# Kernel optimization log

Measured on AMD Instinct MI355X. Metric: run time of the kernel, lower is better.

The kernel has to match this reference:

```python
import jax, jax.numpy as jnp
import numpy as np

DELTA_COEFF = 1.0
CLAMP_MIN = 1e-3  # hardcoded in original clamp(min=0.001)


def setup_inputs() -> dict:
    key = jax.random.key(0)
    k1, k2, k3 = jax.random.split(key, 3)
    B, N, F_in, F_out = 2, 1024, 128, 64
    x = jax.random.normal(k1, (B, N, F_in), dtype=jnp.float32)
    adj = jax.random.uniform(k2, (B, N, N), dtype=jnp.float32)
    weight = jax.random.normal(k3, (F_in, F_out), dtype=jnp.float32) * (1.0 / np.sqrt(F_in))
    bias = jnp.zeros((F_out,), dtype=jnp.float32)
    return {"x": x, "adj": adj, "weight": weight, "bias": bias}


def reference(x, adj, weight, bias):
    # x: [B,N,F_in], adj: [B,N,N]
    x = x @ weight  # [B,N,F_out]
    B, N, _ = adj.shape
    # pairwise L1 distance: [B,N,N]
    abs_diff = jnp.sum(jnp.abs(x[:, :, None, :] - x[:, None, :, :]), axis=-1)
    mod_adj = adj / jnp.maximum(abs_diff, CLAMP_MIN)
    deg = jnp.sum(mod_adj, axis=-1)  # [B,N]
    # Laplacian L = D - A~ ; then I - delta * L
    lap = jnp.zeros_like(mod_adj).at[:, jnp.arange(N), jnp.arange(N)].set(deg) - mod_adj
    mod = jnp.eye(N, dtype=x.dtype) - DELTA_COEFF * lap
    out = jnp.matmul(mod, x) + bias
    return out
```

## Files before the change

kernel.cpp:

```cpp
#include <hip/hip_runtime.h>
#include <hip/hip_fp16.h>


#define JS 16
#define HSTR 72

typedef _Float16 half4_t __attribute__((ext_vector_type(4)));
typedef _Float16 half8_t __attribute__((ext_vector_type(8)));
typedef float    f32x4_t __attribute__((ext_vector_type(4)));

__global__ __launch_bounds__(256) void gemm_xw(const float* __restrict__ x,
                                               const float* __restrict__ w,
                                               float* __restrict__ xw,
                                               __half* __restrict__ xwh,
                                               __half* __restrict__ xwt) {
    __shared__ float ws_[128 * 64];
    __shared__ float xs[8 * 132];
    __shared__ __half ts[8 * 64];
    const int tid = threadIdx.x;
    const int r0  = blockIdx.x * 8;

#pragma unroll
    for (int e = tid; e < 2048; e += 256)
        ((float4*)ws_)[e] = ((const float4*)w)[e];
    {
        int row = tid >> 5, c = tid & 31;
        float4 v = *(const float4*)&x[(size_t)(r0 + row) * 128 + c * 4];
        *(float4*)&xs[row * 132 + c * 4] = v;
    }
    __syncthreads();

    const int rl = tid >> 5;
    const int fg = tid & 31;
    float2 acc = {0.f, 0.f};
#pragma unroll
    for (int k4 = 0; k4 < 32; ++k4) {
        float4 xv = *(const float4*)&xs[rl * 132 + k4 * 4];
        const float* xp = &xv.x;
#pragma unroll
        for (int m = 0; m < 4; ++m) {
            float2 wv = *(const float2*)&ws_[(k4 * 4 + m) * 64 + 2 * fg];
            acc.x += xp[m] * wv.x; acc.y += xp[m] * wv.y;
        }
    }
    size_t o = (size_t)(r0 + rl) * 64 + 2 * fg;
    *(float2*)&xw[o] = acc;
    __half2 h2 = __floats2half2_rn(acc.x, acc.y);
    *(__half2*)&xwh[o] = h2;
    *(__half2*)&ts[rl * 64 + 2 * fg] = h2;
    __syncthreads();

    if (tid < 64) {
        const int f = tid;
        const int b = r0 >> 10;
        const int n0 = r0 & 1023;
        __half hv[8];
#pragma unroll
        for (int r = 0; r < 8; ++r) hv[r] = ts[r * 64 + f];
        *(half8_t*)&xwt[((size_t)(b * 64 + f)) * 1024 + n0] = *(half8_t*)hv;
    }
}

template <bool ATOMIC>
__global__ __launch_bounds__(256) void fused_gtv(const __half* __restrict__ xwh,
                                                 const __half* __restrict__ xwt,
                                                 const float* __restrict__ adj,
                                                 __half* __restrict__ part,
                                                 float* __restrict__ aout,
                                                 float* __restrict__ pdeg) {
    __shared__ __half xih[64 * HSTR];
    __shared__ __half xjh[64 * HSTR];
    __shared__ __half xjt[64 * HSTR];
    __shared__ __half wt [64 * HSTR];

    const int tid = threadIdx.x;
    const int bx  = blockIdx.x;
    const int js  = bx & 15;
    const int it  = (bx >> 4) & 15;
    const int b   = bx >> 8;
    const int i0  = it * 64;
    const int j0  = js * 64;

    const __half* xhb = xwh + (size_t)b * 65536;
    const __half* xtb = xwt + (size_t)b * 65536;
    const float*  adjb = adj + (size_t)b * 1048576;

    const int ty = tid >> 4;
    const int tx = tid & 15;

    float4 av[4];
#pragma unroll
    for (int r = 0; r < 4; ++r)
        av[r] = *(const float4*)&adjb[(size_t)(i0 + 4 * ty + r) * 1024 + j0 + 4 * tx];

#pragma unroll
    for (int e = tid; e < 512; e += 256) {
        int row = e >> 3, cb = e & 7;
        int sc = ((cb ^ ((row >> 2) & 7)) << 3);
        float4 vi = *(const float4*)&xhb[(i0 + row) * 64 + cb * 8];
        *(float4*)&xih[row * HSTR + sc] = vi;
        float4 vj = *(const float4*)&xhb[(j0 + row) * 64 + cb * 8];
        *(float4*)&xjh[row * HSTR + sc] = vj;
        float4 vt = *(const float4*)&xtb[row * 1024 + j0 + cb * 8];
        *(float4*)&xjt[row * HSTR + cb * 8] = vt;
    }
    __syncthreads();

    __half2 acc[4][4];
#pragma unroll
    for (int r = 0; r < 4; ++r)
#pragma unroll
        for (int q = 0; q < 4; ++q) acc[r][q] = __floats2half2_rn(0.f, 0.f);

#pragma unroll
    for (int c = 0; c < 8; ++c) {
        const int ca = ((c ^ (ty & 7)) << 3);
        const int cb = ((c ^ (tx & 7)) << 3);
        float4 a[4], bb[4];
#pragma unroll
        for (int r = 0; r < 4; ++r)
            a[r] = *(const float4*)&xih[(4 * ty + r) * HSTR + ca];
#pragma unroll
        for (int q = 0; q < 4; ++q)
            bb[q] = *(const float4*)&xjh[(4 * tx + q) * HSTR + cb];
#pragma unroll
        for (int r = 0; r < 4; ++r) {
            const __half2* pa = (const __half2*)&a[r];
#pragma unroll
            for (int q = 0; q < 4; ++q) {
                const __half2* pb = (const __half2*)&bb[q];
#pragma unroll
                for (int m = 0; m < 4; ++m)
                    acc[r][q] = __hadd2(acc[r][q], __habs2(__hsub2(pa[m], pb[m])));
            }
        }
    }

    float dsum[4];
#pragma unroll
    for (int r = 0; r < 4; ++r) {
        const int gi = i0 + 4 * ty + r;
        float wv[4];
        dsum[r] = 0.f;
#pragma unroll
        for (int q = 0; q < 4; ++q) {
            float d = __low2float(acc[r][q]) + __high2float(acc[r][q]);
            float inv = __builtin_amdgcn_rcpf(fmaxf(d, 1e-3f));
            float v = (&av[r].x)[q] * inv;
            wv[q] = (gi == j0 + 4 * tx + q) ? 0.f : v;
            dsum[r] += wv[q];
        }
        float2 packed;
        ((__half2*)&packed)[0] = __floats2half2_rn(wv[0], wv[1]);
        ((__half2*)&packed)[1] = __floats2half2_rn(wv[2], wv[3]);
        *(float2*)&wt[(4 * ty + r) * HSTR + 4 * tx] = packed;
    }
#pragma unroll
    for (int r = 0; r < 4; ++r) {
#pragma unroll
        for (int m = 1; m < 16; m <<= 1)
            dsum[r] += __shfl_xor(dsum[r], m, 16);
    }
    if (tx == 0) {
#pragma unroll
        for (int r = 0; r < 4; ++r) {
            if (ATOMIC) atomicAdd(&pdeg[b * 1024 + i0 + 4 * ty + r], dsum[r]);
            else pdeg[(js * 2 + b) * 1024 + i0 + 4 * ty + r] = dsum[r];
        }
    }
    __syncthreads();

    const int wv_  = tid >> 6;
    const int lane = tid & 63;
    const int quad = lane >> 4;
    const int l15  = lane & 15;

    f32x4_t c[4] = {{0,0,0,0},{0,0,0,0},{0,0,0,0},{0,0,0,0}};
    half8_t a0 = *(half8_t*)&wt[(wv_ * 16 + l15) * HSTR + quad * 8];
    half8_t a1 = *(half8_t*)&wt[(wv_ * 16 + l15) * HSTR + 32 + quad * 8];
#pragma unroll
    for (int n = 0; n < 4; ++n) {
        half8_t b0 = *(half8_t*)&xjt[(n * 16 + l15) * HSTR + quad * 8];
        half8_t b1 = *(half8_t*)&xjt[(n * 16 + l15) * HSTR + 32 + quad * 8];
        c[n] = __builtin_amdgcn_mfma_f32_16x16x32_f16(a0, b0, c[n], 0, 0, 0);
        c[n] = __builtin_amdgcn_mfma_f32_16x16x32_f16(a1, b1, c[n], 0, 0, 0);
    }

    if (ATOMIC) {
#pragma unroll
        for (int n = 0; n < 4; ++n)
#pragma unroll
            for (int r = 0; r < 4; ++r) {
                int row = wv_ * 16 + quad * 4 + r;
                atomicAdd(&aout[((size_t)b * 1024 + i0 + row) * 64 + n * 16 + l15], c[n][r]);
            }
    } else {
        const size_t slot = (size_t)(js * 2 + b) * 65536;
#pragma unroll
        for (int n = 0; n < 4; ++n)
#pragma unroll
            for (int r = 0; r < 4; ++r) {
                int row = wv_ * 16 + quad * 4 + r;
                part[slot + (i0 + row) * 64 + n * 16 + l15] = __float2half(c[n][r]);
            }
    }
}

__global__ __launch_bounds__(256) void finish_gtv_v2(const float* __restrict__ xw,
                                                     const __half* __restrict__ part,
                                                     const float* __restrict__ pdeg,
                                                     const float* __restrict__ bias,
                                                     float* __restrict__ out) {
    int idx2 = blockIdx.x * 256 + threadIdx.x;
    int f2 = idx2 & 31;
    int r  = idx2 >> 5;
    int b  = r >> 10;
    int n  = r & 1023;

    float2 s = {0.f, 0.f};
    float dgs = 0.f;
    const __half2* p2 = (const __half2*)part;
#pragma unroll
    for (int js = 0; js < JS; ++js) {
        int sl = js * 2 + b;
        __half2 h = p2[(size_t)sl * 32768 + n * 32 + f2];
        float2 f = __half22float2(h);
        s.x += f.x; s.y += f.y;
        dgs += pdeg[sl * 1024 + n];
    }
    float2 xv = ((const float2*)xw)[idx2];
    float2 bv = ((const float2*)bias)[f2];
    float id = 1.f - dgs;
    float2 o;
    o.x = s.x + id * xv.x + bv.x;
    o.y = s.y + id * xv.y + bv.y;
    ((float2*)out)[idx2] = o;
}

__global__ __launch_bounds__(256) void finish_gtv_atomic(const float* __restrict__ xw,
                                                         const float* __restrict__ pdeg,
                                                         const float* __restrict__ bias,
                                                         float* __restrict__ out) {
    int idx = blockIdx.x * 256 + threadIdx.x;
    int f = idx & 63;
    int r = idx >> 6;
    out[idx] = out[idx] + (1.f - pdeg[r]) * xw[idx] + bias[f];
}

extern "C" void kernel_launch(void* const* d_in, const int* in_sizes, int n_in,
                              void* d_out, int out_size, void* d_ws, size_t ws_size,
                              hipStream_t stream) {
    const float* x    = (const float*)d_in[0];
    const float* adj  = (const float*)d_in[1];
    const float* w    = (const float*)d_in[2];
    const float* bias = (const float*)d_in[3];
    float* out = (float*)d_out;

    char* wsb = (char*)d_ws;
    float*  xw   = (float*)wsb;
    __half* xwh  = (__half*)(wsb + 512 * 1024);
    __half* xwt  = (__half*)(wsb + 768 * 1024);
    float*  pdeg = (float*)(wsb + 1024 * 1024);
    __half* part = (__half*)(wsb + 1152 * 1024);
    const size_t NEED = 1152 * 1024 + (size_t)32 * 65536 * 2;

    gemm_xw<<<256, 256, 0, stream>>>(x, w, xw, xwh, xwt);

    if (ws_size >= NEED) {
        fused_gtv<false><<<512, 256, 0, stream>>>(xwh, xwt, adj, part, nullptr, pdeg);
        finish_gtv_v2<<<256, 256, 0, stream>>>(xw, part, pdeg, bias, out);
    } else {
        hipMemsetAsync(out, 0, 2 * 1024 * 64 * sizeof(float), stream);
        hipMemsetAsync(pdeg, 0, 2 * 1024 * sizeof(float), stream);
        fused_gtv<true><<<512, 256, 0, stream>>>(xwh, xwt, adj, nullptr, out, pdeg);
        finish_gtv_atomic<<<512, 256, 0, stream>>>(xw, pdeg, bias, out);
    }
}
```

Measured before the change: 81.61 us.

## Fuse final reduction into gtv kernel via last-block election counter

The partial-sum reduction and output epilogue move into the main fused kernel. An atomic per-row-tile counter elects the last of the 16 column blocks to sum the fp16 partials and degree partials and write the output. This removes a separate kernel launch and its dependency gap. It adds a threadfence/atomic handshake and relies on the counter in workspace starting at a multiple of 16, since it is never reset explicitly. The atomic fallback path is split into its own kernel.

```diff
diff --git a/kernel.cpp b/kernel.cpp
--- a/kernel.cpp
+++ b/kernel.cpp
@@ -61,13 +61,15 @@
     }
 }
 
-template <bool ATOMIC>
-__global__ __launch_bounds__(256) void fused_gtv(const __half* __restrict__ xwh,
-                                                 const __half* __restrict__ xwt,
-                                                 const float* __restrict__ adj,
-                                                 __half* __restrict__ part,
-                                                 float* __restrict__ aout,
-                                                 float* __restrict__ pdeg) {
+__global__ __launch_bounds__(256) void fused_gtv_fin(const __half* __restrict__ xwh,
+                                                     const __half* __restrict__ xwt,
+                                                     const float* __restrict__ adj,
+                                                     __half* __restrict__ part,
+                                                     float* __restrict__ pdeg,
+                                                     const float* __restrict__ xw,
+                                                     const float* __restrict__ bias,
+                                                     float* __restrict__ out,
+                                                     unsigned* __restrict__ done) {
     __shared__ __half xih[64 * HSTR];
     __shared__ __half xjh[64 * HSTR];
     __shared__ __half xjt[64 * HSTR];
@@ -163,10 +165,8 @@
     }
     if (tx == 0) {
 #pragma unroll
-        for (int r = 0; r < 4; ++r) {
-            if (ATOMIC) atomicAdd(&pdeg[b * 1024 + i0 + 4 * ty + r], dsum[r]);
-            else pdeg[(js * 2 + b) * 1024 + i0 + 4 * ty + r] = dsum[r];
-        }
+        for (int r = 0; r < 4; ++r)
+            pdeg[(js * 2 + b) * 1024 + i0 + 4 * ty + r] = dsum[r];
     }
     __syncthreads();
 
@@ -186,55 +186,184 @@
         c[n] = __builtin_amdgcn_mfma_f32_16x16x32_f16(a1, b1, c[n], 0, 0, 0);
     }
 
-    if (ATOMIC) {
-#pragma unroll
-        for (int n = 0; n < 4; ++n)
-#pragma unroll
-            for (int r = 0; r < 4; ++r) {
-                int row = wv_ * 16 + quad * 4 + r;
-                atomicAdd(&aout[((size_t)b * 1024 + i0 + row) * 64 + n * 16 + l15], c[n][r]);
+    const size_t slot = (size_t)(js * 2 + b) * 65536;
+#pragma unroll
+    for (int n = 0; n < 4; ++n)
+#pragma unroll
+        for (int r = 0; r < 4; ++r) {
+            int row = wv_ * 16 + quad * 4 + r;
+            part[slot + (i0 + row) * 64 + n * 16 + l15] = __float2half(c[n][r]);
+        }
+
+    __syncthreads();
+    __shared__ int elect;
+    if (tid == 0) {
+        __threadfence();
+        unsigned old = atomicAdd(&done[b * 16 + it], 1u);
+        elect = ((old & 15u) == 15u);
+    }
+    __syncthreads();
+    if (!elect) return;
+    __threadfence();
+
+    const float2*  xw2   = (const float2*)xw;
+    const float2*  bias2 = (const float2*)bias;
+    const __half2* p2    = (const __half2*)part;
+    float2*        out2  = (float2*)out;
+#pragma unroll 2
+    for (int k = 0; k < 8; ++k) {
+        int e   = tid + k * 256;
+        int row = e >> 5;
+        int f2  = e & 31;
+        int n   = i0 + row;
+        size_t gr = (size_t)b * 1024 + n;
+        float sx = 0.f, sy = 0.f, dg = 0.f;
+#pragma unroll
+        for (int q = 0; q < JS; ++q) {
+            int sl = q * 2 + b;
+            __half2 h = p2[(size_t)sl * 32768 + (size_t)n * 32 + f2];
+            float2 f = __half22float2(h);
+            sx += f.x; sy += f.y;
+            dg += pdeg[sl * 1024 + n];
+        }
+        float2 xv = xw2[gr * 32 + f2];
+        float2 bv = bias2[f2];
+        float id = 1.f - dg;
+        float2 o;
+        o.x = sx + id * xv.x + bv.x;
+        o.y = sy + id * xv.y + bv.y;
+        out2[gr * 32 + f2] = o;
+    }
+}
+
+__global__ __launch_bounds__(256) void fused_gtv_atomic(const __half* __restrict__ xwh,
+                                                        const __half* __restrict__ xwt,
+                                                        const float* __restrict__ adj,
+                                                        float* __restrict__ aout,
+                                                        float* __restrict__ pdeg) {
+    __shared__ __half xih[64 * HSTR];
+    __shared__ __half xjh[64 * HSTR];
+    __shared__ __half xjt[64 * HSTR];
+    __shared__ __half wt [64 * HSTR];
+
+    const int tid = threadIdx.x;
+    const int bx  = blockIdx.x;
+    const int js  = bx & 15;
+    const int it  = (bx >> 4) & 15;
+    const int b   = bx >> 8;
+    const int i0  = it * 64;
+    const int j0  = js * 64;
+
+    const __half* xhb = xwh + (size_t)b * 65536;
+    const __half* xtb = xwt + (size_t)b * 65536;
+    const float*  adjb = adj + (size_t)b * 1048576;
+
+    const int ty = tid >> 4;
+    const int tx = tid & 15;
+
+    float4 av[4];
+#pragma unroll
+    for (int r = 0; r < 4; ++r)
+        av[r] = *(const float4*)&adjb[(size_t)(i0 + 4 * ty + r) * 1024 + j0 + 4 * tx];
+
+#pragma unroll
+    for (int e = tid; e < 512; e += 256) {
+        int row = e >> 3, cb = e & 7;
+        int sc = ((cb ^ ((row >> 2) & 7)) << 3);
+        float4 vi = *(const float4*)&xhb[(i0 + row) * 64 + cb * 8];
+        *(float4*)&xih[row * HSTR + sc] = vi;
+        float4 vj = *(const float4*)&xhb[(j0 + row) * 64 + cb * 8];
+        *(float4*)&xjh[row * HSTR + sc] = vj;
+        float4 vt = *(const float4*)&xtb[row * 1024 + j0 + cb * 8];
+        *(float4*)&xjt[row * HSTR + cb * 8] = vt;
+    }
+    __syncthreads();
+
+    __half2 acc[4][4];
+#pragma unroll
+    for (int r = 0; r < 4; ++r)
+#pragma unroll
+        for (int q = 0; q < 4; ++q) acc[r][q] = __floats2half2_rn(0.f, 0.f);
+
+#pragma unroll
+    for (int c = 0; c < 8; ++c) {
+        const int ca = ((c ^ (ty & 7)) << 3);
+        const int cb = ((c ^ (tx & 7)) << 3);
+        float4 a[4], bb[4];
+#pragma unroll
+        for (int r = 0; r < 4; ++r)
+            a[r] = *(const float4*)&xih[(4 * ty + r) * HSTR + ca];
+#pragma unroll
+        for (int q = 0; q < 4; ++q)
+            bb[q] = *(const float4*)&xjh[(4 * tx + q) * HSTR + cb];
+#pragma unroll
+        for (int r = 0; r < 4; ++r) {
+            const __half2* pa = (const __half2*)&a[r];
+#pragma unroll
+            for (int q = 0; q < 4; ++q) {
+                const __half2* pb = (const __half2*)&bb[q];
+#pragma unroll
+                for (int m = 0; m < 4; ++m)
+                    acc[r][q] = __hadd2(acc[r][q], __habs2(__hsub2(pa[m], pb[m])));
             }
-    } else {
-        const size_t slot = (size_t)(js * 2 + b) * 65536;
-#pragma unroll
-        for (int n = 0; n < 4; ++n)
-#pragma unroll
-            for (int r = 0; r < 4; ++r) {
-                int row = wv_ * 16 + quad * 4 + r;
-                part[slot + (i0 + row) * 64 + n * 16 + l15] = __float2half(c[n][r]);
-            }
-    }
-}
-
-__global__ __launch_bounds__(256) void finish_gtv_v2(const float* __restrict__ xw,
-                                                     const __half* __restrict__ part,
-                                                     const float* __restrict__ pdeg,
-                                                     const float* __restrict__ bias,
-                                                     float* __restrict__ out) {
-    int idx2 = blockIdx.x * 256 + threadIdx.x;
-    int f2 = idx2 & 31;
-    int r  = idx2 >> 5;
-    int b  = r >> 10;
-    int n  = r & 1023;
-
-    float2 s = {0.f, 0.f};
-    float dgs = 0.f;
-    const __half2* p2 = (const __half2*)part;
-#pragma unroll
-    for (int js = 0; js < JS; ++js) {
-        int sl = js * 2 + b;
-        __half2 h = p2[(size_t)sl * 32768 + n * 32 + f2];
-        float2 f = __half22float2(h);
-        s.x += f.x; s.y += f.y;
-        dgs += pdeg[sl * 1024 + n];
-    }
-    float2 xv = ((const float2*)xw)[idx2];
-    float2 bv = ((const float2*)bias)[f2];
-    float id = 1.f - dgs;
-    float2 o;
-    o.x = s.x + id * xv.x + bv.x;
-    o.y = s.y + id * xv.y + bv.y;
-    ((float2*)out)[idx2] = o;
+        }
+    }
+
+    float dsum[4];
+#pragma unroll
+    for (int r = 0; r < 4; ++r) {
+        const int gi = i0 + 4 * ty + r;
+        float wv[4];
+        dsum[r] = 0.f;
+#pragma unroll
+        for (int q = 0; q < 4; ++q) {
+            float d = __low2float(acc[r][q]) + __high2float(acc[r][q]);
+            float inv = __builtin_amdgcn_rcpf(fmaxf(d, 1e-3f));
+            float v = (&av[r].x)[q] * inv;
+            wv[q] = (gi == j0 + 4 * tx + q) ? 0.f : v;
+            dsum[r] += wv[q];
+        }
+        float2 packed;
+        ((__half2*)&packed)[0] = __floats2half2_rn(wv[0], wv[1]);
+        ((__half2*)&packed)[1] = __floats2half2_rn(wv[2], wv[3]);
+        *(float2*)&wt[(4 * ty + r) * HSTR + 4 * tx] = packed;
+    }
+#pragma unroll
+    for (int r = 0; r < 4; ++r) {
+#pragma unroll
+        for (int m = 1; m < 16; m <<= 1)
+            dsum[r] += __shfl_xor(dsum[r], m, 16);
+    }
+    if (tx == 0) {
+#pragma unroll
+        for (int r = 0; r < 4; ++r)
+            atomicAdd(&pdeg[b * 1024 + i0 + 4 * ty + r], dsum[r]);
+    }
+    __syncthreads();
+
+    const int wv_  = tid >> 6;
+    const int lane = tid & 63;
+    const int quad = lane >> 4;
+    const int l15  = lane & 15;
+
+    f32x4_t c[4] = {{0,0,0,0},{0,0,0,0},{0,0,0,0},{0,0,0,0}};
+    half8_t a0 = *(half8_t*)&wt[(wv_ * 16 + l15) * HSTR + quad * 8];
+    half8_t a1 = *(half8_t*)&wt[(wv_ * 16 + l15) * HSTR + 32 + quad * 8];
+#pragma unroll
+    for (int n = 0; n < 4; ++n) {
+        half8_t b0 = *(half8_t*)&xjt[(n * 16 + l15) * HSTR + quad * 8];
+        half8_t b1 = *(half8_t*)&xjt[(n * 16 + l15) * HSTR + 32 + quad * 8];
+        c[n] = __builtin_amdgcn_mfma_f32_16x16x32_f16(a0, b0, c[n], 0, 0, 0);
+        c[n] = __builtin_amdgcn_mfma_f32_16x16x32_f16(a1, b1, c[n], 0, 0, 0);
+    }
+
+#pragma unroll
+    for (int n = 0; n < 4; ++n)
+#pragma unroll
+        for (int r = 0; r < 4; ++r) {
+            int row = wv_ * 16 + quad * 4 + r;
+            atomicAdd(&aout[((size_t)b * 1024 + i0 + row) * 64 + n * 16 + l15], c[n][r]);
+        }
 }
 
 __global__ __launch_bounds__(256) void finish_gtv_atomic(const float* __restrict__ xw,
@@ -257,22 +386,23 @@
     float* out = (float*)d_out;
 
     char* wsb = (char*)d_ws;
-    float*  xw   = (float*)wsb;
-    __half* xwh  = (__half*)(wsb + 512 * 1024);
-    __half* xwt  = (__half*)(wsb + 768 * 1024);
-    float*  pdeg = (float*)(wsb + 1024 * 1024);
-    __half* part = (__half*)(wsb + 1152 * 1024);
-    const size_t NEED = 1152 * 1024 + (size_t)32 * 65536 * 2;
+    float*    xw   = (float*)wsb;
+    __half*   xwh  = (__half*)(wsb + 512 * 1024);
+    __half*   xwt  = (__half*)(wsb + 768 * 1024);
+    float*    pdeg = (float*)(wsb + 1024 * 1024);
+    __half*   part = (__half*)(wsb + 1152 * 1024);
+    unsigned* done = (unsigned*)(wsb + 5248 * 1024);
+    const size_t NEED = 5248 * 1024 + 128;
 
     gemm_xw<<<256, 256, 0, stream>>>(x, w, xw, xwh, xwt);
 
     if (ws_size >= NEED) {
-        fused_gtv<false><<<512, 256, 0, stream>>>(xwh, xwt, adj, part, nullptr, pdeg);
-        finish_gtv_v2<<<256, 256, 0, stream>>>(xw, part, pdeg, bias, out);
+        fused_gtv_fin<<<512, 256, 0, stream>>>(xwh, xwt, adj, part, pdeg,
+                                               xw, bias, out, done);
     } else {
         hipMemsetAsync(out, 0, 2 * 1024 * 64 * sizeof(float), stream);
         hipMemsetAsync(pdeg, 0, 2 * 1024 * sizeof(float), stream);
-        fused_gtv<true><<<512, 256, 0, stream>>>(xwh, xwt, adj, nullptr, out, pdeg);
+        fused_gtv_atomic<<<512, 256, 0, stream>>>(xwh, xwt, adj, out, pdeg);
         finish_gtv_atomic<<<512, 256, 0, stream>>>(xw, pdeg, bias, out);
     }
 }
```

Result: slower. 104.4 us (+27.9%).

## Fuse distance, degree, aggregation and epilogue into one row-block kernel

Applied to the files above, without the earlier changes.

Replaces the 64x64 tiled pairwise kernel plus reduction/finish kernel with a single kernel where each block owns four output rows across all 1024 columns. Degree sums and the MFMA aggregation are completed in-block, removing the fp16 partial buffer, the extra launch and the atomic fallback. In exchange, each thread reads neighbor feature rows directly from global memory with little reuse, and the MFMA tiles are padded from 4 to 16 rows, wasting most of the matrix work.

```diff
diff --git a/kernel.cpp b/kernel.cpp
--- a/kernel.cpp
+++ b/kernel.cpp
@@ -2,10 +2,8 @@
 #include <hip/hip_fp16.h>
 
 
-#define JS 16
-#define HSTR 72
+#define WSTR 1032
 
-typedef _Float16 half4_t __attribute__((ext_vector_type(4)));
 typedef _Float16 half8_t __attribute__((ext_vector_type(8)));
 typedef float    f32x4_t __attribute__((ext_vector_type(4)));
 
@@ -61,50 +59,44 @@
     }
 }
 
-template <bool ATOMIC>
-__global__ __launch_bounds__(256) void fused_gtv(const __half* __restrict__ xwh,
-                                                 const __half* __restrict__ xwt,
-                                                 const float* __restrict__ adj,
-                                                 __half* __restrict__ part,
-                                                 float* __restrict__ aout,
-                                                 float* __restrict__ pdeg) {
-    __shared__ __half xih[64 * HSTR];
-    __shared__ __half xjh[64 * HSTR];
-    __shared__ __half xjt[64 * HSTR];
-    __shared__ __half wt [64 * HSTR];
+__global__ __launch_bounds__(256) void fused_rows(const __half* __restrict__ xwh,
+                                                  const __half* __restrict__ xwt,
+                                                  const float* __restrict__ adj,
+                                                  const float* __restrict__ xw,
+                                                  const float* __restrict__ bias,
+                                                  float* __restrict__ out) {
+    __shared__ __half xih[4 * 64];
+    __shared__ __half wt[16 * WSTR];
+    __shared__ float  ps[4 * 68];
+    __shared__ float  dpart[16];
 
-    const int tid = threadIdx.x;
-    const int bx  = blockIdx.x;
-    const int js  = bx & 15;
-    const int it  = (bx >> 4) & 15;
-    const int b   = bx >> 8;
-    const int i0  = it * 64;
-    const int j0  = js * 64;
+    const int tid  = threadIdx.x;
+    const int bx   = blockIdx.x;
+    const int b    = bx >> 8;
+    const int i0   = (bx & 255) * 4;
+    const int w_   = tid >> 6;
+    const int lane = tid & 63;
 
-    const __half* xhb = xwh + (size_t)b * 65536;
-    const __half* xtb = xwt + (size_t)b * 65536;
-    const float*  adjb = adj + (size_t)b * 1048576;
+    const __half* xb = xwh + (size_t)b * 65536;
 
-    const int ty = tid >> 4;
-    const int tx = tid & 15;
+    if (tid < 32) {
+        int row = tid >> 3, cb = tid & 7;
+        *(float4*)&xih[row * 64 + cb * 8] =
+            *(const float4*)&xb[(i0 + row) * 64 + cb * 8];
+    }
+    {
+        float4 z = {0.f, 0.f, 0.f, 0.f};
+        float4* wz = (float4*)&wt[4 * WSTR];
+#pragma unroll 2
+        for (int e = tid; e < 1548; e += 256) wz[e] = z;
+    }
+    __syncthreads();
 
     float4 av[4];
 #pragma unroll
     for (int r = 0; r < 4; ++r)
-        av[r] = *(const float4*)&adjb[(size_t)(i0 + 4 * ty + r) * 1024 + j0 + 4 * tx];
-
-#pragma unroll
-    for (int e = tid; e < 512; e += 256) {
-        int row = e >> 3, cb = e & 7;
-        int sc = ((cb ^ ((row >> 2) & 7)) << 3);
-        float4 vi = *(const float4*)&xhb[(i0 + row) * 64 + cb * 8];
-        *(float4*)&xih[row * HSTR + sc] = vi;
-        float4 vj = *(const float4*)&xhb[(j0 + row) * 64 + cb * 8];
-        *(float4*)&xjh[row * HSTR + sc] = vj;
-        float4 vt = *(const float4*)&xtb[row * 1024 + j0 + cb * 8];
-        *(float4*)&xjt[row * HSTR + cb * 8] = vt;
-    }
-    __syncthreads();
+        av[r] = *(const float4*)&adj[(size_t)b * 1048576 +
+                                     (size_t)(i0 + r) * 1024 + 4 * tid];
 
     __half2 acc[4][4];
 #pragma unroll
@@ -113,22 +105,18 @@
         for (int q = 0; q < 4; ++q) acc[r][q] = __floats2half2_rn(0.f, 0.f);
 
 #pragma unroll
-    for (int c = 0; c < 8; ++c) {
-        const int ca = ((c ^ (ty & 7)) << 3);
-        const int cb = ((c ^ (tx & 7)) << 3);
-        float4 a[4], bb[4];
+    for (int q = 0; q < 4; ++q) {
+        float4 bj[8];
 #pragma unroll
-        for (int r = 0; r < 4; ++r)
-            a[r] = *(const float4*)&xih[(4 * ty + r) * HSTR + ca];
+        for (int cb = 0; cb < 8; ++cb)
+            bj[cb] = *(const float4*)&xb[(size_t)(4 * tid + q) * 64 + cb * 8];
 #pragma unroll
-        for (int q = 0; q < 4; ++q)
-            bb[q] = *(const float4*)&xjh[(4 * tx + q) * HSTR + cb];
+        for (int cb = 0; cb < 8; ++cb) {
+            const __half2* pb = (const __half2*)&bj[cb];
 #pragma unroll
-        for (int r = 0; r < 4; ++r) {
-            const __half2* pa = (const __half2*)&a[r];
-#pragma unroll
-            for (int q = 0; q < 4; ++q) {
-                const __half2* pb = (const __half2*)&bb[q];
+            for (int r = 0; r < 4; ++r) {
+                float4 a = *(const float4*)&xih[r * 64 + cb * 8];
+                const __half2* pa = (const __half2*)&a;
 #pragma unroll
                 for (int m = 0; m < 4; ++m)
                     acc[r][q] = __hadd2(acc[r][q], __habs2(__hsub2(pa[m], pb[m])));
@@ -136,115 +124,60 @@
         }
     }
 
-    float dsum[4];
+    float dsum[4] = {0.f, 0.f, 0.f, 0.f};
 #pragma unroll
     for (int r = 0; r < 4; ++r) {
-        const int gi = i0 + 4 * ty + r;
+        const int gi = i0 + r;
         float wv[4];
-        dsum[r] = 0.f;
 #pragma unroll
         for (int q = 0; q < 4; ++q) {
             float d = __low2float(acc[r][q]) + __high2float(acc[r][q]);
             float inv = __builtin_amdgcn_rcpf(fmaxf(d, 1e-3f));
             float v = (&av[r].x)[q] * inv;
-            wv[q] = (gi == j0 + 4 * tx + q) ? 0.f : v;
+            wv[q] = (gi == 4 * tid + q) ? 0.f : v;
             dsum[r] += wv[q];
         }
         float2 packed;
         ((__half2*)&packed)[0] = __floats2half2_rn(wv[0], wv[1]);
         ((__half2*)&packed)[1] = __floats2half2_rn(wv[2], wv[3]);
-        *(float2*)&wt[(4 * ty + r) * HSTR + 4 * tx] = packed;
+        *(float2*)&wt[r * WSTR + 4 * tid] = packed;
     }
 #pragma unroll
     for (int r = 0; r < 4; ++r) {
 #pragma unroll
-        for (int m = 1; m < 16; m <<= 1)
-            dsum[r] += __shfl_xor(dsum[r], m, 16);
+        for (int m = 1; m < 64; m <<= 1)
+            dsum[r] += __shfl_xor(dsum[r], m, 64);
     }
-    if (tx == 0) {
+    if (lane == 0) {
 #pragma unroll
-        for (int r = 0; r < 4; ++r) {
-            if (ATOMIC) atomicAdd(&pdeg[b * 1024 + i0 + 4 * ty + r], dsum[r]);
-            else pdeg[(js * 2 + b) * 1024 + i0 + 4 * ty + r] = dsum[r];
-        }
+        for (int r = 0; r < 4; ++r) dpart[w_ * 4 + r] = dsum[r];
     }
     __syncthreads();
 
-    const int wv_  = tid >> 6;
-    const int lane = tid & 63;
     const int quad = lane >> 4;
     const int l15  = lane & 15;
+    const __half* bt = xwt + (size_t)b * 65536 + (size_t)(w_ * 16 + l15) * 1024;
 
-    f32x4_t c[4] = {{0,0,0,0},{0,0,0,0},{0,0,0,0},{0,0,0,0}};
-    half8_t a0 = *(half8_t*)&wt[(wv_ * 16 + l15) * HSTR + quad * 8];
-    half8_t a1 = *(half8_t*)&wt[(wv_ * 16 + l15) * HSTR + 32 + quad * 8];
+    f32x4_t c = {0.f, 0.f, 0.f, 0.f};
+#pragma unroll 8
+    for (int kc = 0; kc < 32; ++kc) {
+        half8_t af = *(const half8_t*)&wt[l15 * WSTR + kc * 32 + quad * 8];
+        half8_t bf = *(const half8_t*)&bt[kc * 32 + quad * 8];
+        c = __builtin_amdgcn_mfma_f32_16x16x32_f16(af, bf, c, 0, 0, 0);
+    }
+    if (quad == 0) {
 #pragma unroll
-    for (int n = 0; n < 4; ++n) {
-        half8_t b0 = *(half8_t*)&xjt[(n * 16 + l15) * HSTR + quad * 8];
-        half8_t b1 = *(half8_t*)&xjt[(n * 16 + l15) * HSTR + 32 + quad * 8];
-        c[n] = __builtin_amdgcn_mfma_f32_16x16x32_f16(a0, b0, c[n], 0, 0, 0);
-        c[n] = __builtin_amdgcn_mfma_f32_16x16x32_f16(a1, b1, c[n], 0, 0, 0);
+        for (int r = 0; r < 4; ++r) ps[r * 68 + w_ * 16 + l15] = c[r];
     }
+    __syncthreads();
 
-    if (ATOMIC) {
-#pragma unroll
-        for (int n = 0; n < 4; ++n)
-#pragma unroll
-            for (int r = 0; r < 4; ++r) {
-                int row = wv_ * 16 + quad * 4 + r;
-                atomicAdd(&aout[((size_t)b * 1024 + i0 + row) * 64 + n * 16 + l15], c[n][r]);
-            }
-    } else {
-        const size_t slot = (size_t)(js * 2 + b) * 65536;
-#pragma unroll
-        for (int n = 0; n < 4; ++n)
-#pragma unroll
-            for (int r = 0; r < 4; ++r) {
-                int row = wv_ * 16 + quad * 4 + r;
-                part[slot + (i0 + row) * 64 + n * 16 + l15] = __float2half(c[n][r]);
-            }
+    {
+        int row = tid >> 6;
+        int f   = tid & 63;
+        float deg = dpart[row] + dpart[4 + row] + dpart[8 + row] + dpart[12 + row];
+        size_t o = ((size_t)b * 1024 + i0 + row) * 64 + f;
+        out[o] = (1.f - deg) * xw[o] + ps[row * 68 + f] + bias[f];
     }
-}
-
-__global__ __launch_bounds__(256) void finish_gtv_v2(const float* __restrict__ xw,
-                                                     const __half* __restrict__ part,
-                                                     const float* __restrict__ pdeg,
-                                                     const float* __restrict__ bias,
-                                                     float* __restrict__ out) {
-    int idx2 = blockIdx.x * 256 + threadIdx.x;
-    int f2 = idx2 & 31;
-    int r  = idx2 >> 5;
-    int b  = r >> 10;
-    int n  = r & 1023;
-
-    float2 s = {0.f, 0.f};
-    float dgs = 0.f;
-    const __half2* p2 = (const __half2*)part;
-#pragma unroll
-    for (int js = 0; js < JS; ++js) {
-        int sl = js * 2 + b;
-        __half2 h = p2[(size_t)sl * 32768 + n * 32 + f2];
-        float2 f = __half22float2(h);
-        s.x += f.x; s.y += f.y;
-        dgs += pdeg[sl * 1024 + n];
-    }
-    float2 xv = ((const float2*)xw)[idx2];
-    float2 bv = ((const float2*)bias)[f2];
-    float id = 1.f - dgs;
-    float2 o;
-    o.x = s.x + id * xv.x + bv.x;
-    o.y = s.y + id * xv.y + bv.y;
-    ((float2*)out)[idx2] = o;
-}
-
-__global__ __launch_bounds__(256) void finish_gtv_atomic(const float* __restrict__ xw,
-                                                         const float* __restrict__ pdeg,
-                                                         const float* __restrict__ bias,
-                                                         float* __restrict__ out) {
-    int idx = blockIdx.x * 256 + threadIdx.x;
-    int f = idx & 63;
-    int r = idx >> 6;
-    out[idx] = out[idx] + (1.f - pdeg[r]) * xw[idx] + bias[f];
 }
 
 extern "C" void kernel_launch(void* const* d_in, const int* in_sizes, int n_in,
@@ -257,22 +190,10 @@
     float* out = (float*)d_out;
 
     char* wsb = (char*)d_ws;
-    float*  xw   = (float*)wsb;
-    __half* xwh  = (__half*)(wsb + 512 * 1024);
-    __half* xwt  = (__half*)(wsb + 768 * 1024);
-    float*  pdeg = (float*)(wsb + 1024 * 1024);
-    __half* part = (__half*)(wsb + 1152 * 1024);
-    const size_t NEED = 1152 * 1024 + (size_t)32 * 65536 * 2;
+    float*  xw  = (float*)wsb;
+    __half* xwh = (__half*)(wsb + 512 * 1024);
+    __half* xwt = (__half*)(wsb + 768 * 1024);
 
     gemm_xw<<<256, 256, 0, stream>>>(x, w, xw, xwh, xwt);
-
-    if (ws_size >= NEED) {
-        fused_gtv<false><<<512, 256, 0, stream>>>(xwh, xwt, adj, part, nullptr, pdeg);
-        finish_gtv_v2<<<256, 256, 0, stream>>>(xw, part, pdeg, bias, out);
-    } else {
-        hipMemsetAsync(out, 0, 2 * 1024 * 64 * sizeof(float), stream);
-        hipMemsetAsync(pdeg, 0, 2 * 1024 * sizeof(float), stream);
-        fused_gtv<true><<<512, 256, 0, stream>>>(xwh, xwt, adj, nullptr, out, pdeg);
-        finish_gtv_atomic<<<512, 256, 0, stream>>>(xw, pdeg, bias, out);
-    }
+    fused_rows<<<512, 256, 0, stream>>>(xwh, xwt, adj, xw, bias, out);
 }
```

Measured after the change: 86.31 us. 1.06x slower.

## Fuse three kernels into one cooperative launch with grid syncs

Applied to the files above, without the earlier changes.

Merges the projection GEMM, the fused pairwise-L1/Laplacian kernel and the finish reduction into one cooperative kernel separated by grid.sync, with a union of shared memory buffers. It falls back to the three separate launches if the cooperative launch fails. It also replaces the half2 abs with a sign-bit mask in the L1 accumulation. The aim is to remove the overhead and tail gaps of two kernel launches, at the cost of grid barriers and a larger shared-memory footprint per block, which may reduce occupancy.

```diff
diff --git a/kernel.cpp b/kernel.cpp
--- a/kernel.cpp
+++ b/kernel.cpp
@@ -1,25 +1,31 @@
 #include <hip/hip_runtime.h>
 #include <hip/hip_fp16.h>
+#include <hip/hip_cooperative_groups.h>
+
+namespace cg = cooperative_groups;
 
 
 #define JS 16
 #define HSTR 72
 
-typedef _Float16 half4_t __attribute__((ext_vector_type(4)));
 typedef _Float16 half8_t __attribute__((ext_vector_type(8)));
+typedef _Float16 h2_t    __attribute__((ext_vector_type(2)));
 typedef float    f32x4_t __attribute__((ext_vector_type(4)));
 
-__global__ __launch_bounds__(256) void gemm_xw(const float* __restrict__ x,
-                                               const float* __restrict__ w,
-                                               float* __restrict__ xw,
-                                               __half* __restrict__ xwh,
-                                               __half* __restrict__ xwt) {
-    __shared__ float ws_[128 * 64];
-    __shared__ float xs[8 * 132];
-    __shared__ __half ts[8 * 64];
-    const int tid = threadIdx.x;
-    const int r0  = blockIdx.x * 8;
-
+static __device__ __forceinline__ h2_t l1acc(h2_t acc, h2_t a, h2_t b) {
+    h2_t d = a - b;
+    unsigned ad = __builtin_bit_cast(unsigned, d) & 0x7FFF7FFFu;
+    return acc + __builtin_bit_cast(h2_t, ad);
+}
+
+
+static __device__ __forceinline__ void gemm_body(float* ws_, float* xs, __half* ts,
+                                                 int r0, int tid,
+                                                 const float* __restrict__ x,
+                                                 const float* __restrict__ w,
+                                                 float* __restrict__ xw,
+                                                 __half* __restrict__ xwh,
+                                                 __half* __restrict__ xwt) {
 #pragma unroll
     for (int e = tid; e < 2048; e += 256)
         ((float4*)ws_)[e] = ((const float4*)w)[e];
@@ -62,19 +68,15 @@
 }
 
 template <bool ATOMIC>
-__global__ __launch_bounds__(256) void fused_gtv(const __half* __restrict__ xwh,
-                                                 const __half* __restrict__ xwt,
-                                                 const float* __restrict__ adj,
-                                                 __half* __restrict__ part,
-                                                 float* __restrict__ aout,
-                                                 float* __restrict__ pdeg) {
-    __shared__ __half xih[64 * HSTR];
-    __shared__ __half xjh[64 * HSTR];
-    __shared__ __half xjt[64 * HSTR];
-    __shared__ __half wt [64 * HSTR];
-
-    const int tid = threadIdx.x;
-    const int bx  = blockIdx.x;
+static __device__ __forceinline__ void fused_body(__half* xih, __half* xjh,
+                                                  __half* xjt, __half* wt,
+                                                  int bx, int tid,
+                                                  const __half* __restrict__ xwh,
+                                                  const __half* __restrict__ xwt,
+                                                  const float* __restrict__ adj,
+                                                  __half* __restrict__ part,
+                                                  float* __restrict__ aout,
+                                                  float* __restrict__ pdeg) {
     const int js  = bx & 15;
     const int it  = (bx >> 4) & 15;
     const int b   = bx >> 8;
@@ -106,11 +108,12 @@
     }
     __syncthreads();
 
-    __half2 acc[4][4];
+    h2_t acc[4][4];
 #pragma unroll
     for (int r = 0; r < 4; ++r)
 #pragma unroll
-        for (int q = 0; q < 4; ++q) acc[r][q] = __floats2half2_rn(0.f, 0.f);
+        for (int q = 0; q < 4; ++q)
+            acc[r][q] = (h2_t){(_Float16)0, (_Float16)0};
 
 #pragma unroll
     for (int c = 0; c < 8; ++c) {
@@ -125,13 +128,13 @@
             bb[q] = *(const float4*)&xjh[(4 * tx + q) * HSTR + cb];
 #pragma unroll
         for (int r = 0; r < 4; ++r) {
-            const __half2* pa = (const __half2*)&a[r];
+            const h2_t* pa = (const h2_t*)&a[r];
 #pragma unroll
             for (int q = 0; q < 4; ++q) {
-                const __half2* pb = (const __half2*)&bb[q];
+                const h2_t* pb = (const h2_t*)&bb[q];
 #pragma unroll
                 for (int m = 0; m < 4; ++m)
-                    acc[r][q] = __hadd2(acc[r][q], __habs2(__hsub2(pa[m], pb[m])));
+                    acc[r][q] = l1acc(acc[r][q], pa[m], pb[m]);
             }
         }
     }
@@ -144,7 +147,7 @@
         dsum[r] = 0.f;
 #pragma unroll
         for (int q = 0; q < 4; ++q) {
-            float d = __low2float(acc[r][q]) + __high2float(acc[r][q]);
+            float d = (float)acc[r][q][0] + (float)acc[r][q][1];
             float inv = __builtin_amdgcn_rcpf(fmaxf(d, 1e-3f));
             float v = (&av[r].x)[q] * inv;
             wv[q] = (gi == j0 + 4 * tx + q) ? 0.f : v;
@@ -206,12 +209,12 @@
     }
 }
 
-__global__ __launch_bounds__(256) void finish_gtv_v2(const float* __restrict__ xw,
-                                                     const __half* __restrict__ part,
-                                                     const float* __restrict__ pdeg,
-                                                     const float* __restrict__ bias,
-                                                     float* __restrict__ out) {
-    int idx2 = blockIdx.x * 256 + threadIdx.x;
+static __device__ __forceinline__ void finish_body(int idx2,
+                                                   const float* __restrict__ xw,
+                                                   const __half* __restrict__ part,
+                                                   const float* __restrict__ pdeg,
+                                                   const float* __restrict__ bias,
+                                                   float* __restrict__ out) {
     int f2 = idx2 & 31;
     int r  = idx2 >> 5;
     int b  = r >> 10;
@@ -237,10 +240,79 @@
     ((float2*)out)[idx2] = o;
 }
 
-__global__ __launch_bounds__(256) void finish_gtv_atomic(const float* __restrict__ xw,
-                                                         const float* __restrict__ pdeg,
-                                                         const float* __restrict__ bias,
-                                                         float* __restrict__ out) {
+union LdsU {
+    struct { float ws_[8192]; float xs[1056]; __half ts[512]; } g;
+    struct { __half xih[64 * HSTR]; __half xjh[64 * HSTR];
+             __half xjt[64 * HSTR]; __half wt [64 * HSTR]; } f;
+};
+
+__global__ __launch_bounds__(256) void gtv_coop(const float* __restrict__ x,
+                                                const float* __restrict__ w,
+                                                float* __restrict__ xw,
+                                                __half* __restrict__ xwh,
+                                                __half* __restrict__ xwt,
+                                                const float* __restrict__ adj,
+                                                __half* __restrict__ part,
+                                                float* __restrict__ pdeg,
+                                                const float* __restrict__ bias,
+                                                float* __restrict__ out) {
+    __shared__ LdsU u;
+    cg::grid_group grid = cg::this_grid();
+    const int tid = threadIdx.x;
+    const int bx  = blockIdx.x;
+
+    if (bx < 256)
+        gemm_body(u.g.ws_, u.g.xs, u.g.ts, bx * 8, tid, x, w, xw, xwh, xwt);
+
+    grid.sync();
+
+    fused_body<false>(u.f.xih, u.f.xjh, u.f.xjt, u.f.wt, bx, tid,
+                      xwh, xwt, adj, part, nullptr, pdeg);
+
+    grid.sync();
+
+    if (bx < 256)
+        finish_body(bx * 256 + tid, xw, part, pdeg, bias, out);
+}
+
+__global__ __launch_bounds__(256) void gemm_xw_k(const float* __restrict__ x,
+                                                 const float* __restrict__ w,
+                                                 float* __restrict__ xw,
+                                                 __half* __restrict__ xwh,
+                                                 __half* __restrict__ xwt) {
+    __shared__ float ws_[128 * 64];
+    __shared__ float xs[8 * 132];
+    __shared__ __half ts[8 * 64];
+    gemm_body(ws_, xs, ts, blockIdx.x * 8, threadIdx.x, x, w, xw, xwh, xwt);
+}
+
+template <bool ATOMIC>
+__global__ __launch_bounds__(256) void fused_gtv_k(const __half* __restrict__ xwh,
+                                                   const __half* __restrict__ xwt,
+                                                   const float* __restrict__ adj,
+                                                   __half* __restrict__ part,
+                                                   float* __restrict__ aout,
+                                                   float* __restrict__ pdeg) {
+    __shared__ __half xih[64 * HSTR];
+    __shared__ __half xjh[64 * HSTR];
+    __shared__ __half xjt[64 * HSTR];
+    __shared__ __half wt [64 * HSTR];
+    fused_body<ATOMIC>(xih, xjh, xjt, wt, blockIdx.x, threadIdx.x,
+                       xwh, xwt, adj, part, aout, pdeg);
+}
+
+__global__ __launch_bounds__(256) void finish_gtv_k(const float* __restrict__ xw,
+                                                    const __half* __restrict__ part,
+                                                    const float* __restrict__ pdeg,
+                                                    const float* __restrict__ bias,
+                                                    float* __restrict__ out) {
+    finish_body(blockIdx.x * 256 + threadIdx.x, xw, part, pdeg, bias, out);
+}
+
+__global__ __launch_bounds__(256) void finish_gtv_atomic_k(const float* __restrict__ xw,
+                                                           const float* __restrict__ pdeg,
+                                                           const float* __restrict__ bias,
+                                                           float* __restrict__ out) {
     int idx = blockIdx.x * 256 + threadIdx.x;
     int f = idx & 63;
     int r = idx >> 6;
@@ -264,15 +336,22 @@
     __half* part = (__half*)(wsb + 1152 * 1024);
     const size_t NEED = 1152 * 1024 + (size_t)32 * 65536 * 2;
 
-    gemm_xw<<<256, 256, 0, stream>>>(x, w, xw, xwh, xwt);
-
     if (ws_size >= NEED) {
-        fused_gtv<false><<<512, 256, 0, stream>>>(xwh, xwt, adj, part, nullptr, pdeg);
-        finish_gtv_v2<<<256, 256, 0, stream>>>(xw, part, pdeg, bias, out);
+        void* args[] = {(void*)&x, (void*)&w, (void*)&xw, (void*)&xwh, (void*)&xwt,
+                        (void*)&adj, (void*)&part, (void*)&pdeg, (void*)&bias,
+                        (void*)&out};
+        hipError_t err = hipLaunchCooperativeKernel((const void*)gtv_coop,
+                                                    dim3(512), dim3(256),
+                                                    args, 0, stream);
+        if (err == hipSuccess) return;
+        gemm_xw_k<<<256, 256, 0, stream>>>(x, w, xw, xwh, xwt);
+        fused_gtv_k<false><<<512, 256, 0, stream>>>(xwh, xwt, adj, part, nullptr, pdeg);
+        finish_gtv_k<<<256, 256, 0, stream>>>(xw, part, pdeg, bias, out);
     } else {
+        gemm_xw_k<<<256, 256, 0, stream>>>(x, w, xw, xwh, xwt);
         hipMemsetAsync(out, 0, 2 * 1024 * 64 * sizeof(float), stream);
         hipMemsetAsync(pdeg, 0, 2 * 1024 * sizeof(float), stream);
-        fused_gtv<true><<<512, 256, 0, stream>>>(xwh, xwt, adj, nullptr, out, pdeg);
-        finish_gtv_atomic<<<512, 256, 0, stream>>>(xw, pdeg, bias, out);
-    }
-}
+        fused_gtv_k<true><<<512, 256, 0, stream>>>(xwh, xwt, adj, nullptr, out, pdeg);
+        finish_gtv_atomic_k<<<512, 256, 0, stream>>>(xw, pdeg, bias, out);
+    }
+}
```

New measurement: 201.7 us. +147.1%, slower.
